# Optimization experiments

Measured on AMD Instinct MI355X. Metric: run time of the kernel, lower is better.

## Reference

```python
import jax, jax.numpy as jnp
import numpy as np

B, H, P, D, NF = 16, 12, 256, 64, 8  # batch, heads, patches, head_dim, num_f


def setup_inputs() -> dict:
    key = jax.random.key(0)
    ks = jax.random.split(key, 8)
    q = jax.random.normal(ks[0], (B, H, P, D), dtype=jnp.float32)
    k = jax.random.normal(ks[1], (B, H, P, D), dtype=jnp.float32)
    scale = jnp.ones((1,), dtype=jnp.float32)  # accepted but unused by forward
    grid = jnp.arange(NF, dtype=jnp.float32) + 1.0  # nn.Parameter(arange(num_f)+1)
    base_weight = jax.random.uniform(ks[2], (D, D), dtype=jnp.float32)  # torch.rand
    coef = jax.random.uniform(ks[3], (D, NF), dtype=jnp.float32)
    scale_base = jnp.ones((1, H, P, D), dtype=jnp.float32)
    scale_sp = jnp.ones((1, H, P, D), dtype=jnp.float32)
    # tiny lin_qk init so matrix_exp of the P x P logits stays finite
    a = 1e-3
    lin_w = jax.random.uniform(ks[4], (P, P), dtype=jnp.float32, minval=-a, maxval=a)
    lin_b = jax.random.uniform(ks[5], (P,), dtype=jnp.float32, minval=-a, maxval=a)
    return {"q": q, "k": k, "scale": scale, "grid": grid, "base_weight": base_weight,
            "coef": coef, "scale_base": scale_base, "scale_sp": scale_sp,
            "lin_w": lin_w, "lin_b": lin_b}


def reference(q, k, scale, grid, base_weight, coef, scale_base, scale_sp, lin_w, lin_b):
    def sig_rowsum(x):
        # F.linear(silu(x), base_weight): x @ base_weight.T
        base = jax.nn.silu(x) @ base_weight.T                       # [B,H,P,D]
        # KAN sin basis: sum_f coef[d,f] * sin(grid[f] * x[...,d])
        f = jnp.einsum('bhpdf,df->bhpd', jnp.sin(x[..., None] * grid), coef)
        f = f * scale_sp + base * scale_base                        # [B,H,P,D]
        # sigmoid(fq)[p,:,d] + sigmoid(fk)[:,p',d] summed over d is separable:
        return jax.nn.sigmoid(f).sum(axis=-1)                       # [B,H,P]

    sq = sig_rowsum(q)
    sk = sig_rowsum(k)
    f_out = sq[..., :, None] + sk[..., None, :]                     # [B,H,P,P]
    f_out = f_out @ lin_w.T + lin_b                                 # lin_qk over last dim
    E = jax.vmap(jax.scipy.linalg.expm)(f_out.reshape(-1, P, P)).reshape(B, H, P, P)
    k_new = E @ k                                                   # [B,H,P,D]
    return (q, k_new)
```

## Files before the change

### kernel.cpp

```cpp
#include <hip/hip_runtime.h>
#include <hip/hip_bf16.h>
#include <math.h>

constexpr int KB_B  = 16;
constexpr int KB_H  = 12;
constexpr int KB_P  = 256;
constexpr int KB_D  = 64;
constexpr int KB_NROWS = KB_B * KB_H * KB_P;
constexpr int KB_QBLOCKS = KB_NROWS / 64;

typedef __bf16 bf16x8 __attribute__((ext_vector_type(8)));
typedef float  f32x4  __attribute__((ext_vector_type(4)));

__device__ inline float ka_sigmoid(float v) {
    return __builtin_amdgcn_rcpf(1.f + __expf(-v));
}
__device__ inline __bf16 ka_silu_bf(float f) {
    return (__bf16)(f * ka_sigmoid(f));
}

__global__ __launch_bounds__(256, 4) void ka_sig_rowsum(
    const float* __restrict__ q, const float* __restrict__ k,
    const float* __restrict__ bw, const float* __restrict__ coef,
    float* __restrict__ sq, float* __restrict__ sk, float* __restrict__ out_q)
{
    const int tid  = threadIdx.x;
    const int lane = tid & 63;
    const int wv   = tid >> 6;
    const int l15  = lane & 15;
    const int lg   = lane >> 4;

    const bool is_q = blockIdx.x < KB_QBLOCKS;
    const int  blk  = is_q ? blockIdx.x : blockIdx.x - KB_QBLOCKS;
    const float* __restrict__ x    = is_q ? q : k;
    float* __restrict__       outp = is_q ? sq : sk;
    const size_t tile_f = (size_t)blk * 4096;

    if (is_q) {
        const f32x4* xin = reinterpret_cast<const f32x4*>(x + tile_f);
        f32x4* qout = reinterpret_cast<f32x4*>(out_q + tile_f);
#pragma unroll
        for (int c = 0; c < 4; ++c) qout[c * 256 + tid] = xin[c * 256 + tid];
    }

    bf16x8 afrag[2];
    {
        const float* xp = x + tile_f + (size_t)(wv * 16 + l15) * KB_D + 8 * lg;
#pragma unroll
        for (int h = 0; h < 2; ++h) {
            f32x4 p0 = *reinterpret_cast<const f32x4*>(xp + 32 * h);
            f32x4 p1 = *reinterpret_cast<const f32x4*>(xp + 32 * h + 4);
#pragma unroll
            for (int j = 0; j < 4; ++j) {
                afrag[h][j]     = ka_silu_bf(p0[j]);
                afrag[h][j + 4] = ka_silu_bf(p1[j]);
            }
        }
    }

    f32x4 acc[4];
#pragma unroll
    for (int nt = 0; nt < 4; ++nt) {
        const float* bp = bw + (nt * 16 + l15) * KB_D + 8 * lg;
        bf16x8 bfrag[2];
#pragma unroll
        for (int h = 0; h < 2; ++h) {
            f32x4 p0 = *reinterpret_cast<const f32x4*>(bp + 32 * h);
            f32x4 p1 = *reinterpret_cast<const f32x4*>(bp + 32 * h + 4);
#pragma unroll
            for (int j = 0; j < 4; ++j) {
                bfrag[h][j]     = (__bf16)p0[j];
                bfrag[h][j + 4] = (__bf16)p1[j];
            }
        }
        acc[nt] = (f32x4){0.f, 0.f, 0.f, 0.f};
        acc[nt] = __builtin_amdgcn_mfma_f32_16x16x32_bf16(afrag[0], bfrag[0], acc[nt], 0, 0, 0);
        acc[nt] = __builtin_amdgcn_mfma_f32_16x16x32_bf16(afrag[1], bfrag[1], acc[nt], 0, 0, 0);
    }

    const int arow = wv * 16 + lg * 4;
    float rowsum[4] = {0.f, 0.f, 0.f, 0.f};

#pragma unroll
    for (int nt = 0; nt < 4; ++nt) {
        const int d = nt * 16 + l15;
        f32x4 c0 = *reinterpret_cast<const f32x4*>(coef + d * 8);
        f32x4 c1 = *reinterpret_cast<const f32x4*>(coef + d * 8 + 4);
#pragma unroll
        for (int reg = 0; reg < 4; ++reg) {
            const int row = arow + reg;
            const float xv = x[tile_f + (size_t)row * KB_D + d];
            const float s1 = __sinf(xv);
            const float tc = 2.f * __cosf(xv);
            float fk = c0[0] * s1;
            float spp = 0.f, sp_ = s1;
#pragma unroll
            for (int n = 1; n < 8; ++n) {
                const float sn = tc * sp_ - spp;
                const float cn = (n < 4) ? c0[n] : c1[n - 4];
                fk = fmaf(cn, sn, fk);
                spp = sp_; sp_ = sn;
            }
            rowsum[reg] += ka_sigmoid(fk + acc[nt][reg]);
        }
    }

#pragma unroll
    for (int reg = 0; reg < 4; ++reg) {
        float s = rowsum[reg];
        s += __shfl_xor(s, 1);
        s += __shfl_xor(s, 2);
        s += __shfl_xor(s, 4);
        s += __shfl_xor(s, 8);
        if (l15 == 0) outp[blk * 64 + arow + reg] = s;
    }
}

__global__ __launch_bounds__(256, 4) void ka_partials(
    const float* __restrict__ k, const float* __restrict__ lin_w,
    const float* __restrict__ lin_b, const float* __restrict__ sq,
    const float* __restrict__ sk,
    float* __restrict__ t1p, float* __restrict__ t2p, float* __restrict__ s_part)
{
    const int bh = blockIdx.x >> 2;
    const int ch = blockIdx.x & 3;
    const int t  = threadIdx.x;
    const int lane = t & 63;
    const int wv   = t >> 6;

    __shared__ float sk_sh[KB_P];
    __shared__ float vpart[64][68];
    __shared__ float rpart[64][68];
    __shared__ float rv_sh[2][64];
    __shared__ float t1sh[4][64], t2sh[4][64];

    sk_sh[t] = sk[bh * KB_P + t];
    __syncthreads();

    const f32x4* wf4 = reinterpret_cast<const f32x4*>(lin_w + (size_t)ch * 64 * KB_P);
#pragma unroll 4
    for (int c = 0; c < 16; ++c) {
        const f32x4 w = wf4[c * 256 + t];
        const f32x4 s4 = *reinterpret_cast<const f32x4*>(&sk_sh[lane * 4]);
        vpart[c * 4 + wv][lane] = w[0]*s4[0] + w[1]*s4[1] + w[2]*s4[2] + w[3]*s4[3];
        rpart[c * 4 + wv][lane] = (w[0] + w[1]) + (w[2] + w[3]);
    }
    __syncthreads();

    if (t < 64) {
        float vs = 0.f, rs = 0.f;
#pragma unroll
        for (int g = 0; g < 16; ++g) {
            f32x4 a = *reinterpret_cast<const f32x4*>(&vpart[t][g * 4]);
            f32x4 b = *reinterpret_cast<const f32x4*>(&rpart[t][g * 4]);
            vs += (a[0] + a[1]) + (a[2] + a[3]);
            rs += (b[0] + b[1]) + (b[2] + b[3]);
        }
        rv_sh[0][t] = rs;
        rv_sh[1][t] = vs + lin_b[ch * 64 + t];
    }
    __syncthreads();

    if (wv == 0) {
        const float a = sq[bh * KB_P + ch * 64 + lane];
        const float r = rv_sh[0][lane];
        const float v = rv_sh[1][lane];
        float d0 = r * a, d1 = r, d2 = v * a, d3 = v;
#pragma unroll
        for (int off = 32; off; off >>= 1) {
            d0 += __shfl_down(d0, off);
            d1 += __shfl_down(d1, off);
            d2 += __shfl_down(d2, off);
            d3 += __shfl_down(d3, off);
        }
        if (lane == 0) {
            float* spo = s_part + (bh * 4 + ch) * 4;
            spo[0] = d0; spo[1] = d1; spo[2] = d2; spo[3] = d3;
        }
    }

    const float* kc = k + ((size_t)bh * KB_P + ch * 64) * KB_D;
    float t1 = 0.f, t2 = 0.f;
#pragma unroll
    for (int i = 0; i < 16; ++i) {
        const int p = wv * 16 + i;
        const float kv = kc[(size_t)p * KB_D + lane];
        t1 = fmaf(rv_sh[0][p], kv, t1);
        t2 = fmaf(rv_sh[1][p], kv, t2);
    }
    t1sh[wv][lane] = t1;
    t2sh[wv][lane] = t2;
    __syncthreads();

    if (t < 64) {
        t1p[(bh * 4 + ch) * 64 + t] = t1sh[0][t] + t1sh[1][t] + t1sh[2][t] + t1sh[3][t];
        t2p[(bh * 4 + ch) * 64 + t] = t2sh[0][t] + t2sh[1][t] + t2sh[2][t] + t2sh[3][t];
    }
}

__device__ inline double ka_phi_fe(double z) {
    if (fabs(z) < 1e-5)
        return 1.0 + z * (0.5 + z * (1.0 / 6.0 + z * (1.0 / 24.0)));
    return ((double)__expf((float)z) - 1.0) / z;
}
__device__ inline double ka_phip_fe(double z) {
    if (fabs(z) < 1e-4)
        return 0.5 + z * (1.0 / 3.0 + z * 0.125);
    const double e = (double)__expf((float)z);
    return (e * (z - 1.0) + 1.0) / (z * z);
}

__global__ __launch_bounds__(256, 8) void ka_apply(
    const float* __restrict__ k, const float* __restrict__ sq,
    const float* __restrict__ t1p, const float* __restrict__ t2p,
    const float* __restrict__ s_part, float* __restrict__ out_k)
{
    const int bh = blockIdx.x >> 2;
    const int ch = blockIdx.x & 2 ? (blockIdx.x & 3) : (blockIdx.x & 3);
    const int t  = threadIdx.x;
    const int lane = t & 63;
    const int wv   = t >> 6;
    const int c16  = lane & 15;
    const int rg   = lane >> 4;

    const float* sp = s_part + bh * 16;
    const double s11 = (double)sp[0] + sp[4] + sp[8]  + sp[12];
    const double s12 = (double)sp[1] + sp[5] + sp[9]  + sp[13];
    const double s21 = (double)sp[2] + sp[6] + sp[10] + sp[14];
    const double s22 = (double)sp[3] + sp[7] + sp[11] + sp[15];

    const double tr  = s11 + s22;
    const double det = s11 * s22 - s12 * s21;
    const double mu  = 0.5 * tr;
    const double disc = mu * mu - det;
    const double aw  = sqrt(fabs(disc));
    double alpha, beta;
    if (aw < 1e-2) {
        beta  = ka_phip_fe(mu);
        alpha = ka_phi_fe(mu) - beta * mu;
    } else if (disc > 0.0) {
        const double l1 = mu + aw, l2 = mu - aw;
        const double p1 = ka_phi_fe(l1), p2 = ka_phi_fe(l2);
        beta  = (p1 - p2) / (2.0 * aw);
        alpha = p1 - beta * l1;
    } else {
        const double em = (double)__expf((float)mu);
        const double cw = (double)__cosf((float)aw);
        const double sw = (double)__sinf((float)aw);
        const double nre = em * cw - 1.0;
        const double nim = em * sw;
        const double den = mu * mu + aw * aw;
        const double pre = (nre * mu + nim * aw) / den;
        const double pim = (nim * mu - nre * aw) / den;
        beta  = pim / aw;
        alpha = pre - beta * mu;
    }
    const float G00 = (float)(alpha + beta * s11);
    const float G01 = (float)(beta * s12);
    const float G10 = (float)(beta * s21);
    const float G11 = (float)(alpha + beta * s22);

    const int d0 = c16 * 4;
    f32x4 t1v = {0.f, 0.f, 0.f, 0.f}, t2v = {0.f, 0.f, 0.f, 0.f};
#pragma unroll
    for (int c = 0; c < 4; ++c) {
        t1v += *reinterpret_cast<const f32x4*>(t1p + (bh * 4 + c) * 64 + d0);
        t2v += *reinterpret_cast<const f32x4*>(t2p + (bh * 4 + c) * 64 + d0);
    }
    f32x4 y1, y2;
#pragma unroll
    for (int e = 0; e < 4; ++e) {
        y1[e] = G00 * t1v[e] + G01 * t2v[e];
        y2[e] = G10 * t1v[e] + G11 * t2v[e];
    }

    const int prow0 = (blockIdx.x & 3) * 64 + wv * 16;
    const size_t base = ((size_t)bh * KB_P + prow0) * KB_D;
#pragma unroll
    for (int i = 0; i < 4; ++i) {
        const int pr = i * 4 + rg;
        const float a = sq[bh * KB_P + prow0 + pr];
        const f32x4 kv = *reinterpret_cast<const f32x4*>(k + base + (size_t)pr * KB_D + d0);
        f32x4 o;
#pragma unroll
        for (int e = 0; e < 4; ++e) o[e] = fmaf(a, y1[e], kv[e] + y2[e]);
        *reinterpret_cast<f32x4*>(out_k + base + (size_t)pr * KB_D + d0) = o;
    }
}

extern "C" void kernel_launch(void* const* d_in, const int* in_sizes, int n_in,
                              void* d_out, int out_size, void* d_ws, size_t ws_size,
                              hipStream_t stream) {
    const float* q     = (const float*)d_in[0];
    const float* k     = (const float*)d_in[1];
    const float* bw    = (const float*)d_in[4];
    const float* coef  = (const float*)d_in[5];
    const float* lin_w = (const float*)d_in[8];
    const float* lin_b = (const float*)d_in[9];

    float* out = (float*)d_out;
    const size_t tensor_elems = (size_t)KB_B * KB_H * KB_P * KB_D;

    float* sq  = (float*)d_ws;
    float* sk  = sq + KB_NROWS;
    float* t1p = sk + KB_NROWS;
    float* t2p = t1p + KB_NROWS;
    float* spt = t2p + KB_NROWS;

    ka_sig_rowsum<<<2 * KB_QBLOCKS, 256, 0, stream>>>(
        q, k, bw, coef, sq, sk, out);

    ka_partials<<<KB_B * KB_H * 4, 256, 0, stream>>>(
        k, lin_w, lin_b, sq, sk, t1p, t2p, spt);

    ka_apply<<<KB_B * KB_H * 4, 256, 0, stream>>>(
        k, sq, t1p, t2p, spt, out + tensor_elems);
}
```

Before: 36.00 us.

## Fuse partials and apply kernels with per-head atomic barrier, hoist lin_w row sums

Merges the partials and apply kernels into one launch. The four blocks of each batch-head synchronise through an atomic counter and spin-wait before computing the 2x2 exponential and writing out k. Row sums of lin_w, which do not depend on the input, are now computed once by four extra blocks in the first kernel instead of by every block, and those same blocks zero the flags. This removes one kernel launch and the redundant row-sum work, but the spin barrier assumes all four blocks of a head are resident at the same time and adds atomic traffic.

```diff
diff --git a/kernel.cpp b/kernel.cpp
--- a/kernel.cpp
+++ b/kernel.cpp
@@ -22,11 +22,30 @@
 __global__ __launch_bounds__(256, 4) void ka_sig_rowsum(
     const float* __restrict__ q, const float* __restrict__ k,
     const float* __restrict__ bw, const float* __restrict__ coef,
-    float* __restrict__ sq, float* __restrict__ sk, float* __restrict__ out_q)
+    const float* __restrict__ lin_w,
+    float* __restrict__ sq, float* __restrict__ sk,
+    float* __restrict__ r_out, int* __restrict__ flags,
+    float* __restrict__ out_q)
 {
     const int tid  = threadIdx.x;
     const int lane = tid & 63;
     const int wv   = tid >> 6;
+
+    if (blockIdx.x >= 2 * KB_QBLOCKS) {
+        const int b = blockIdx.x - 2 * KB_QBLOCKS;
+        if (tid < 48) flags[b * 48 + tid] = 0;
+        const f32x4* wf4 = reinterpret_cast<const f32x4*>(lin_w);
+#pragma unroll 4
+        for (int c = 0; c < 16; ++c) {
+            f32x4 w = wf4[b * 4096 + c * 256 + tid];
+            float rp = (w[0] + w[1]) + (w[2] + w[3]);
+#pragma unroll
+            for (int off = 32; off; off >>= 1) rp += __shfl_down(rp, off);
+            if (lane == 0) r_out[b * 64 + c * 4 + wv] = rp;
+        }
+        return;
+    }
+
     const int l15  = lane & 15;
     const int lg   = lane >> 4;
 
@@ -116,11 +135,25 @@
     }
 }
 
-__global__ __launch_bounds__(256, 4) void ka_partials(
+__device__ inline double ka_phi_fe(double z) {
+    if (fabs(z) < 1e-5)
+        return 1.0 + z * (0.5 + z * (1.0 / 6.0 + z * (1.0 / 24.0)));
+    return ((double)__expf((float)z) - 1.0) / z;
+}
+__device__ inline double ka_phip_fe(double z) {
+    if (fabs(z) < 1e-4)
+        return 0.5 + z * (1.0 / 3.0 + z * 0.125);
+    const double e = (double)__expf((float)z);
+    return (e * (z - 1.0) + 1.0) / (z * z);
+}
+
+__global__ __launch_bounds__(256, 4) void ka_rank2_fused(
     const float* __restrict__ k, const float* __restrict__ lin_w,
     const float* __restrict__ lin_b, const float* __restrict__ sq,
-    const float* __restrict__ sk,
-    float* __restrict__ t1p, float* __restrict__ t2p, float* __restrict__ s_part)
+    const float* __restrict__ sk, const float* __restrict__ r_glob,
+    float* __restrict__ t1p, float* __restrict__ t2p,
+    float* __restrict__ s_part, int* __restrict__ flags,
+    float* __restrict__ out_k)
 {
     const int bh = blockIdx.x >> 2;
     const int ch = blockIdx.x & 3;
@@ -130,8 +163,7 @@
 
     __shared__ float sk_sh[KB_P];
     __shared__ float vpart[64][68];
-    __shared__ float rpart[64][68];
-    __shared__ float rv_sh[2][64];
+    __shared__ float v_sh[64];
     __shared__ float t1sh[4][64], t2sh[4][64];
 
     sk_sh[t] = sk[bh * KB_P + t];
@@ -143,28 +175,28 @@
         const f32x4 w = wf4[c * 256 + t];
         const f32x4 s4 = *reinterpret_cast<const f32x4*>(&sk_sh[lane * 4]);
         vpart[c * 4 + wv][lane] = w[0]*s4[0] + w[1]*s4[1] + w[2]*s4[2] + w[3]*s4[3];
-        rpart[c * 4 + wv][lane] = (w[0] + w[1]) + (w[2] + w[3]);
-    }
-    __syncthreads();
-
-    if (t < 64) {
-        float vs = 0.f, rs = 0.f;
-#pragma unroll
-        for (int g = 0; g < 16; ++g) {
-            f32x4 a = *reinterpret_cast<const f32x4*>(&vpart[t][g * 4]);
-            f32x4 b = *reinterpret_cast<const f32x4*>(&rpart[t][g * 4]);
-            vs += (a[0] + a[1]) + (a[2] + a[3]);
-            rs += (b[0] + b[1]) + (b[2] + b[3]);
-        }
-        rv_sh[0][t] = rs;
-        rv_sh[1][t] = vs + lin_b[ch * 64 + t];
+    }
+    __syncthreads();
+
+    {
+        const int row = t >> 2, qt = t & 3;
+        const float* vp = &vpart[row][qt * 16];
+        f32x4 a0 = *reinterpret_cast<const f32x4*>(vp);
+        f32x4 a1 = *reinterpret_cast<const f32x4*>(vp + 4);
+        f32x4 a2 = *reinterpret_cast<const f32x4*>(vp + 8);
+        f32x4 a3 = *reinterpret_cast<const f32x4*>(vp + 12);
+        float vs = ((a0[0]+a0[1])+(a0[2]+a0[3])) + ((a1[0]+a1[1])+(a1[2]+a1[3]))
+                 + ((a2[0]+a2[1])+(a2[2]+a2[3])) + ((a3[0]+a3[1])+(a3[2]+a3[3]));
+        vs += __shfl_xor(vs, 1);
+        vs += __shfl_xor(vs, 2);
+        if (qt == 0) v_sh[row] = vs + lin_b[ch * 64 + row];
     }
     __syncthreads();
 
     if (wv == 0) {
         const float a = sq[bh * KB_P + ch * 64 + lane];
-        const float r = rv_sh[0][lane];
-        const float v = rv_sh[1][lane];
+        const float r = r_glob[ch * 64 + lane];
+        const float v = v_sh[lane];
         float d0 = r * a, d1 = r, d2 = v * a, d3 = v;
 #pragma unroll
         for (int off = 32; off; off >>= 1) {
@@ -180,48 +212,39 @@
     }
 
     const float* kc = k + ((size_t)bh * KB_P + ch * 64) * KB_D;
-    float t1 = 0.f, t2 = 0.f;
-#pragma unroll
-    for (int i = 0; i < 16; ++i) {
-        const int p = wv * 16 + i;
-        const float kv = kc[(size_t)p * KB_D + lane];
-        t1 = fmaf(rv_sh[0][p], kv, t1);
-        t2 = fmaf(rv_sh[1][p], kv, t2);
-    }
-    t1sh[wv][lane] = t1;
-    t2sh[wv][lane] = t2;
+    {
+        float t1 = 0.f, t2 = 0.f;
+#pragma unroll
+        for (int i = 0; i < 16; ++i) {
+            const int p = wv * 16 + i;
+            const float kv = kc[(size_t)p * KB_D + lane];
+            t1 = fmaf(r_glob[ch * 64 + p], kv, t1);
+            t2 = fmaf(v_sh[p], kv, t2);
+        }
+        t1sh[wv][lane] = t1;
+        t2sh[wv][lane] = t2;
+    }
     __syncthreads();
 
     if (t < 64) {
         t1p[(bh * 4 + ch) * 64 + t] = t1sh[0][t] + t1sh[1][t] + t1sh[2][t] + t1sh[3][t];
         t2p[(bh * 4 + ch) * 64 + t] = t2sh[0][t] + t2sh[1][t] + t2sh[2][t] + t2sh[3][t];
     }
-}
-
-__device__ inline double ka_phi_fe(double z) {
-    if (fabs(z) < 1e-5)
-        return 1.0 + z * (0.5 + z * (1.0 / 6.0 + z * (1.0 / 24.0)));
-    return ((double)__expf((float)z) - 1.0) / z;
-}
-__device__ inline double ka_phip_fe(double z) {
-    if (fabs(z) < 1e-4)
-        return 0.5 + z * (1.0 / 3.0 + z * 0.125);
-    const double e = (double)__expf((float)z);
-    return (e * (z - 1.0) + 1.0) / (z * z);
-}
-
-__global__ __launch_bounds__(256, 8) void ka_apply(
-    const float* __restrict__ k, const float* __restrict__ sq,
-    const float* __restrict__ t1p, const float* __restrict__ t2p,
-    const float* __restrict__ s_part, float* __restrict__ out_k)
-{
-    const int bh = blockIdx.x >> 2;
-    const int ch = blockIdx.x & 2 ? (blockIdx.x & 3) : (blockIdx.x & 3);
-    const int t  = threadIdx.x;
-    const int lane = t & 63;
-    const int wv   = t >> 6;
-    const int c16  = lane & 15;
-    const int rg   = lane >> 4;
+    __syncthreads();
+
+    if (t == 0) {
+        __threadfence();
+        __hip_atomic_fetch_add(&flags[bh], 1, __ATOMIC_RELEASE,
+                               __HIP_MEMORY_SCOPE_AGENT);
+        int guard = 0;
+        while (__hip_atomic_load(&flags[bh], __ATOMIC_RELAXED,
+                                 __HIP_MEMORY_SCOPE_AGENT) < 4) {
+            __builtin_amdgcn_s_sleep(8);
+            if (++guard > (1 << 27)) break;
+        }
+        __threadfence();
+    }
+    __syncthreads();
 
     const float* sp = s_part + bh * 16;
     const double s11 = (double)sp[0] + sp[4] + sp[8]  + sp[12];
@@ -260,7 +283,9 @@
     const float G10 = (float)(beta * s21);
     const float G11 = (float)(alpha + beta * s22);
 
-    const int d0 = c16 * 4;
+    const int c16 = lane & 15;
+    const int rg  = lane >> 4;
+    const int d0  = c16 * 4;
     f32x4 t1v = {0.f, 0.f, 0.f, 0.f}, t2v = {0.f, 0.f, 0.f, 0.f};
 #pragma unroll
     for (int c = 0; c < 4; ++c) {
@@ -274,7 +299,7 @@
         y2[e] = G10 * t1v[e] + G11 * t2v[e];
     }
 
-    const int prow0 = (blockIdx.x & 3) * 64 + wv * 16;
+    const int prow0 = ch * 64 + wv * 16;
     const size_t base = ((size_t)bh * KB_P + prow0) * KB_D;
 #pragma unroll
     for (int i = 0; i < 4; ++i) {
@@ -306,13 +331,12 @@
     float* t1p = sk + KB_NROWS;
     float* t2p = t1p + KB_NROWS;
     float* spt = t2p + KB_NROWS;
-
-    ka_sig_rowsum<<<2 * KB_QBLOCKS, 256, 0, stream>>>(
-        q, k, bw, coef, sq, sk, out);
-
-    ka_partials<<<KB_B * KB_H * 4, 256, 0, stream>>>(
-        k, lin_w, lin_b, sq, sk, t1p, t2p, spt);
-
-    ka_apply<<<KB_B * KB_H * 4, 256, 0, stream>>>(
-        k, sq, t1p, t2p, spt, out + tensor_elems);
-}
+    int*   flg = (int*)(spt + 3072);
+    float* rws = (float*)(flg + 192);
+
+    ka_sig_rowsum<<<2 * KB_QBLOCKS + 4, 256, 0, stream>>>(
+        q, k, bw, coef, lin_w, sq, sk, rws, flg, out);
+
+    ka_rank2_fused<<<KB_B * KB_H * 4, 256, 0, stream>>>(
+        k, lin_w, lin_b, sq, sk, rws, t1p, t2p, spt, flg, out + tensor_elems);
+}
```

Result: slower. 79.80 us (+121.7%).
